# Performance work log

Hardware: AMD Instinct MI355X
Metric: run time of the kernel (lower is better)

The kernel has to match this reference:

```python
import jax, jax.numpy as jnp
import numpy as np
import math

H = 16
D_MODEL = 1024
LEN_Q = 2048
LEN_K = 2048
D_K = 64
D_V = 64
B = 4
NEG = -1000000000.0


def setup_inputs() -> dict:
    key = jax.random.key(0)
    ks = jax.random.split(key, 9)
    Q = jax.random.normal(ks[0], (B, LEN_Q, D_MODEL), dtype=jnp.float32)
    K = jax.random.normal(ks[1], (B, LEN_K, D_MODEL), dtype=jnp.float32)
    V = jax.random.normal(ks[2], (B, LEN_K, D_MODEL), dtype=jnp.float32)
    mask = jax.random.randint(ks[3], (B, LEN_K), 0, 2, dtype=jnp.int32)
    s = 1.0 / math.sqrt(D_MODEL)
    Wq = jax.random.normal(ks[4], (H * D_K, D_MODEL), dtype=jnp.float32) * s
    bq = jnp.zeros((H * D_K,), dtype=jnp.float32)
    Wk = jax.random.normal(ks[5], (H * D_K, D_MODEL), dtype=jnp.float32) * s
    Wv = jax.random.normal(ks[6], (H * D_V, D_MODEL), dtype=jnp.float32) * s
    bv = jnp.zeros((H * D_V,), dtype=jnp.float32)
    return {"Q": Q, "K": K, "V": V, "mask": mask,
            "Wq": Wq, "bq": bq, "Wk": Wk, "Wv": Wv, "bv": bv}


def reference(Q, K, V, mask, Wq, bq, Wk, Wv, bv):
    scale = math.sqrt(float(D_K))
    # projections (W_Q, W_V have bias; W_K does not)
    q = (jnp.einsum('bsd,od->bso', Q, Wq) + bq).reshape(B, LEN_Q, H, D_K)
    k = jnp.einsum('bsd,od->bso', K, Wk).reshape(B, LEN_K, H, D_K)
    v = (jnp.einsum('bsd,od->bso', V, Wv) + bv).reshape(B, LEN_K, H, D_V)
    # scores [B, H, len_q, len_k]
    A = jnp.einsum('bqhd,bkhd->bhqk', q, k) / scale
    m = (mask != 0)[:, None, None, :]  # [B,1,1,len_k]
    A = jnp.where(m, A, A + 0.0)
    A = jnp.where(m, A, NEG)
    alpha = jax.nn.softmax(A, axis=-1)
    out = jnp.einsum('bhqk,bkhd->bqhd', alpha, v)  # [B, len_q, H, d_v]
    return out.reshape(B, LEN_Q, H * D_V)
```

## Files before the change

### kernel.cpp

```cpp
#include <hip/hip_runtime.h>
#include <stdint.h>
#include <math.h>

#define NH 16
#define DM 1024
#define SEQ 2048
#define DH 64
#define NB 4
#define NEG2 (-1.4426950408889634e9f)
#define SCL2 (0.18033688011112042f)

typedef __attribute__((ext_vector_type(8))) short bf16x8;
typedef __attribute__((ext_vector_type(4))) short bf16x4;
typedef __attribute__((ext_vector_type(4))) float f32x4;
typedef unsigned short u16;
typedef uint32_t u32;

__device__ __forceinline__ u16 f2bf(float f) {
    union { float f; u32 i; } c; c.f = f;
    u32 r = c.i + 0x7fffu + ((c.i >> 16) & 1u);
    return (u16)(r >> 16);
}
__device__ __forceinline__ u32 packbf(float lo, float hi) {
    union { float f; u32 i; } a, b; a.f = lo; b.f = hi;
    return ((a.i + 0x8000u) >> 16) | ((b.i + 0x8000u) & 0xFFFF0000u);
}

__device__ __forceinline__ float fexp2(float x) {
#if __has_builtin(__builtin_amdgcn_exp2f)
    return __builtin_amdgcn_exp2f(x);
#else
    return exp2f(x);
#endif
}

__device__ __forceinline__ f32x4 pv_mfma(bf16x4 a, bf16x4 b, f32x4 c) {
#if __has_builtin(__builtin_amdgcn_mfma_f32_16x16x16bf16_1k)
    return __builtin_amdgcn_mfma_f32_16x16x16bf16_1k(a, b, c, 0, 0, 0);
#else
    f32x4 d;
    asm volatile("s_nop 1\n\t"
                 "v_mfma_f32_16x16x16_bf16 %0, %1, %2, %3\n\t"
                 "s_nop 7\n\t"
                 "s_nop 7"
                 : "=v"(d) : "v"(a), "v"(b), "v"(c));
    return d;
#endif
}

__global__ __launch_bounds__(256) void cvt_kernel(const float* __restrict__ src,
                                                  u16* __restrict__ dst, int n4) {
    int i = blockIdx.x * 256 + threadIdx.x;
    if (i >= n4) return;
    float4 v = ((const float4*)src)[i];
    ushort4 o = { f2bf(v.x), f2bf(v.y), f2bf(v.z), f2bf(v.w) };
    ((ushort4*)dst)[i] = o;
}

__global__ __launch_bounds__(256) void prep_kernel(
    const float* __restrict__ Wq, const float* __restrict__ Wk,
    const float* __restrict__ Wv, const int* __restrict__ mask,
    u16* __restrict__ wqb, u16* __restrict__ wkb, u16* __restrict__ wvb,
    float* __restrict__ mf) {
    const int bid = blockIdx.x;
    if (bid < 3072) {
        const float* src = (bid < 1024) ? Wq : (bid < 2048) ? Wk : Wv;
        u16* dst = (bid < 1024) ? wqb : (bid < 2048) ? wkb : wvb;
        int i = (bid & 1023) * 256 + threadIdx.x;
        float4 v = ((const float4*)src)[i];
        ushort4 o = { f2bf(v.x), f2bf(v.y), f2bf(v.z), f2bf(v.w) };
        ((ushort4*)dst)[i] = o;
    } else {
        int i = (bid - 3072) * 256 + threadIdx.x;
        mf[i] = mask[i] ? 0.0f : NEG2;
    }
}

__global__ __launch_bounds__(256, 3) void proj_kernel(
    const u16* __restrict__ X, const u16* __restrict__ W,
    const float* __restrict__ bias, u16* __restrict__ out, int vt)
{
    __shared__ __align__(16) u16 sbuf[2][8192];
    const int tid  = threadIdx.x;
    const int lane = tid & 63;
    const int wave = tid >> 6;
    const int row  = lane & 15;
    const int quad = lane >> 4;
    const int n0 = blockIdx.x * 128;
    const int m0 = blockIdx.y * 128;
    const int wm = (wave & 1) * 64;
    const int wn = (wave >> 1) * 64;

    const int srow = tid >> 2;
    const int sk8  = (tid & 3) * 8;
    const u16* xg = X + (size_t)(m0 + srow) * DM + sk8;
    const u16* wg = W + (size_t)(n0 + srow) * DM + sk8;
    const int ldsA = tid * 8;
    const int ldsB = 4096 + tid * 8;

    {
        uint4 a0 = *(const uint4*)(xg);
        uint4 a1 = *(const uint4*)(xg + (size_t)64 * DM);
        uint4 b0 = *(const uint4*)(wg);
        uint4 b1 = *(const uint4*)(wg + (size_t)64 * DM);
        *(uint4*)(&sbuf[0][ldsA])        = a0;
        *(uint4*)(&sbuf[0][ldsA + 2048]) = a1;
        *(uint4*)(&sbuf[0][ldsB])        = b0;
        *(uint4*)(&sbuf[0][ldsB + 2048]) = b1;
    }

    f32x4 acc[4][4] = {};
    for (int ki = 0; ki < 32; ++ki) {
        __syncthreads();
        const int ktn = (ki == 31) ? 0 : (ki + 1) * 32;
        uint4 a0 = *(const uint4*)(xg + ktn);
        uint4 a1 = *(const uint4*)(xg + (size_t)64 * DM + ktn);
        uint4 b0 = *(const uint4*)(wg + ktn);
        uint4 b1 = *(const uint4*)(wg + (size_t)64 * DM + ktn);

        const u16* Ab = sbuf[ki & 1];
        const u16* Bb = Ab + 4096;
        bf16x8 af[4], bf[4];
#pragma unroll
        for (int i = 0; i < 4; i++)
            af[i] = *(const bf16x8*)(Ab + (wm + i * 16 + row) * 32 + quad * 8);
#pragma unroll
        for (int j = 0; j < 4; j++)
            bf[j] = *(const bf16x8*)(Bb + (wn + j * 16 + row) * 32 + quad * 8);
#pragma unroll
        for (int i = 0; i < 4; i++)
#pragma unroll
            for (int j = 0; j < 4; j++)
                acc[i][j] = __builtin_amdgcn_mfma_f32_16x16x32_bf16(af[i], bf[j], acc[i][j], 0, 0, 0);

        u16* nb = sbuf[(ki + 1) & 1];
        *(uint4*)(nb + ldsA)        = a0;
        *(uint4*)(nb + ldsA + 2048) = a1;
        *(uint4*)(nb + ldsB)        = b0;
        *(uint4*)(nb + ldsB + 2048) = b1;
    }

    const int bidx = m0 >> 11;
#pragma unroll
    for (int j = 0; j < 4; j++) {
        const int n = n0 + wn + j * 16 + row;
        const int h = n >> 6;
        const int c = n & (DH - 1);
        const float bv = bias ? bias[n] : 0.0f;
#pragma unroll
        for (int i = 0; i < 4; i++) {
            const int mbase = m0 + wm + i * 16 + quad * 4;
            const int s = mbase & (SEQ - 1);
            if (vt) {
                ushort4 o = { f2bf(acc[i][j][0] + bv), f2bf(acc[i][j][1] + bv),
                              f2bf(acc[i][j][2] + bv), f2bf(acc[i][j][3] + bv) };
                size_t idx = (((size_t)(bidx * NH + h) * 32 + (s >> 6)) * DH + c) * 64 + (s & 63);
                *(ushort4*)(out + idx) = o;
            } else {
#pragma unroll
                for (int r = 0; r < 4; r++)
                    out[(size_t)((bidx * NH + h) * SEQ + s + r) * DH + c] = f2bf(acc[i][j][r] + bv);
            }
        }
    }
}

__global__ __launch_bounds__(256, 3) void attn_kernel(
    const u16* __restrict__ qws, const u16* __restrict__ kws,
    const u16* __restrict__ vws, const float* __restrict__ maskf,
    float* __restrict__ out)
{
    __shared__ __align__(16) u16 kbuf[2][64 * 72];
    __shared__ __align__(16) u16 vbuf[2][64 * 72];
    const int tid  = threadIdx.x;
    const int lane = tid & 63;
    const int wave = tid >> 6;
    const int row  = lane & 15;
    const int quad = lane >> 4;
    const int bid = blockIdx.x;
    const int qb = bid & 15;
    const int h  = (bid >> 4) & (NH - 1);
    const int b  = bid >> 8;
    const int q0 = qb * 128 + wave * 32;

    const u16* qbase = qws + (size_t)(b * NH + h) * SEQ * DH;
    const u16* kbase = kws + (size_t)(b * NH + h) * SEQ * DH;
    const u16* vtb   = vws + (size_t)(b * NH + h) * 32 * (DH * 64);
    const float* mrow = maskf + b * SEQ;

    const int srow = tid >> 3;
    const int scol = (tid & 7) * 8;
    const u16* kgp = kbase + (size_t)srow * DH + scol;
    const int ldso = srow * 72 + scol;
    const int vldso = ldso;

    bf16x8 qf[2][2];
#pragma unroll
    for (int gi = 0; gi < 2; gi++) {
        qf[gi][0] = *(const bf16x8*)(qbase + (size_t)(q0 + gi * 16 + row) * DH + quad * 8);
        qf[gi][1] = *(const bf16x8*)(qbase + (size_t)(q0 + gi * 16 + row) * DH + 32 + quad * 8);
    }

    f32x4 O[2][4] = {};
    float lrun[2] = {0.0f, 0.0f};

    {
        uint4 k0 = *(const uint4*)(kgp);
        uint4 k1 = *(const uint4*)(kgp + (size_t)32 * DH);
        uint4 v0 = *(const uint4*)(vtb + tid * 8);
        uint4 v1 = *(const uint4*)(vtb + (tid + 256) * 8);
        *(uint4*)(&kbuf[0][ldso])            = k0;
        *(uint4*)(&kbuf[0][32 * 72 + ldso])  = k1;
        *(uint4*)(&vbuf[0][vldso])           = v0;
        *(uint4*)(&vbuf[0][32 * 72 + vldso]) = v1;
    }

    for (int it = 0; it < 32; ++it) {
        const int kt = it * 64;
        __syncthreads();
        float4 mk[4];
#pragma unroll
        for (int g = 0; g < 4; g++)
            mk[g] = *(const float4*)(mrow + kt + g * 16 + quad * 4);
        const int itn = (it == 31) ? 0 : it + 1;
        uint4 kr0 = *(const uint4*)(kgp + (size_t)itn * 64 * DH);
        uint4 kr1 = *(const uint4*)(kgp + (size_t)(itn * 64 + 32) * DH);
        uint4 vr0 = *(const uint4*)(vtb + (size_t)itn * 4096 + tid * 8);
        uint4 vr1 = *(const uint4*)(vtb + (size_t)itn * 4096 + (tid + 256) * 8);

        const u16* kb = kbuf[it & 1];
        f32x4 st[2][4] = {};
#pragma unroll
        for (int g = 0; g < 4; g++) {
#pragma unroll
            for (int ks = 0; ks < 2; ks++) {
                bf16x8 kf = *(const bf16x8*)(kb + (g * 16 + row) * 72 + ks * 32 + quad * 8);
                st[0][g] = __builtin_amdgcn_mfma_f32_16x16x32_bf16(kf, qf[0][ks], st[0][g], 0, 0, 0);
                st[1][g] = __builtin_amdgcn_mfma_f32_16x16x32_bf16(kf, qf[1][ks], st[1][g], 0, 0, 0);
            }
        }

        union { u32 u[2]; bf16x4 v; } pw[2][4];
#pragma unroll
        for (int gi = 0; gi < 2; gi++) {
            float lsum = 0.0f;
#pragma unroll
            for (int g = 0; g < 4; g++) {
                float p0 = fexp2(fmaf(st[gi][g][0], SCL2, mk[g].x));
                float p1 = fexp2(fmaf(st[gi][g][1], SCL2, mk[g].y));
                float p2 = fexp2(fmaf(st[gi][g][2], SCL2, mk[g].z));
                float p3 = fexp2(fmaf(st[gi][g][3], SCL2, mk[g].w));
                lsum += (p0 + p1) + (p2 + p3);
                pw[gi][g].u[0] = packbf(p0, p1);
                pw[gi][g].u[1] = packbf(p2, p3);
            }
            lsum += __shfl_xor(lsum, 16, 64);
            lsum += __shfl_xor(lsum, 32, 64);
            lrun[gi] += lsum;
        }

        const u16* vb = vbuf[it & 1];
#pragma unroll
        for (int dg = 0; dg < 4; dg++) {
#pragma unroll
            for (int g = 0; g < 4; g++) {
                bf16x4 vfrag = *(const bf16x4*)(vb + (dg * 16 + row) * 72 + g * 16 + quad * 4);
                O[0][dg] = pv_mfma(vfrag, pw[0][g].v, O[0][dg]);
                O[1][dg] = pv_mfma(vfrag, pw[1][g].v, O[1][dg]);
            }
        }

        u16* nkb = kbuf[(it + 1) & 1];
        u16* nvb = vbuf[(it + 1) & 1];
        *(uint4*)(nkb + ldso)             = kr0;
        *(uint4*)(nkb + 32 * 72 + ldso)   = kr1;
        *(uint4*)(nvb + vldso)            = vr0;
        *(uint4*)(nvb + 32 * 72 + vldso)  = vr1;
    }

#pragma unroll
    for (int gi = 0; gi < 2; gi++) {
        const float rl = 1.0f / lrun[gi];
        const int q = q0 + gi * 16 + row;
#pragma unroll
        for (int dg = 0; dg < 4; dg++) {
            float4 o4 = { O[gi][dg][0] * rl, O[gi][dg][1] * rl,
                          O[gi][dg][2] * rl, O[gi][dg][3] * rl };
            *(float4*)(out + (size_t)(b * SEQ + q) * (NH * DH) + h * DH + dg * 16 + quad * 4) = o4;
        }
    }
}

extern "C" void kernel_launch(void* const* d_in, const int* in_sizes, int n_in,
                              void* d_out, int out_size, void* d_ws, size_t ws_size,
                              hipStream_t stream) {
    const float* Q    = (const float*)d_in[0];
    const float* K    = (const float*)d_in[1];
    const float* V    = (const float*)d_in[2];
    const int*   mask = (const int*)d_in[3];
    const float* Wq   = (const float*)d_in[4];
    const float* bq   = (const float*)d_in[5];
    const float* Wk   = (const float*)d_in[6];
    const float* Wv   = (const float*)d_in[7];
    const float* bv   = (const float*)d_in[8];
    float* out = (float*)d_out;

    const size_t XN = (size_t)NB * SEQ * DM;
    const size_t WN = (size_t)DM * DM;
    u16* ws = (u16*)d_ws;
    u16* xbuf = ws;
    u16* wqb  = ws + XN;
    u16* wkb  = wqb + WN;
    u16* wvb  = wkb + WN;
    u16* qws  = wvb + WN;
    u16* kws  = qws + XN;
    u16* vws  = kws + XN;
    float* maskf = (float*)(vws + XN);

    dim3 blk(256);
    const int gX = (int)(XN / 4 / 256);
    prep_kernel<<<3072 + 32, blk, 0, stream>>>(Wq, Wk, Wv, mask, wqb, wkb, wvb, maskf);

    dim3 pgrid(DM / 128, NB * SEQ / 128);
    cvt_kernel<<<gX, blk, 0, stream>>>(Q, xbuf, (int)(XN / 4));
    proj_kernel<<<pgrid, blk, 0, stream>>>(xbuf, wqb, bq, qws, 0);
    cvt_kernel<<<gX, blk, 0, stream>>>(K, xbuf, (int)(XN / 4));
    proj_kernel<<<pgrid, blk, 0, stream>>>(xbuf, wkb, nullptr, kws, 0);
    cvt_kernel<<<gX, blk, 0, stream>>>(V, xbuf, (int)(XN / 4));
    proj_kernel<<<pgrid, blk, 0, stream>>>(xbuf, wvb, bv, vws, 1);

    attn_kernel<<<dim3(NB * NH * (SEQ / 128)), blk, 0, stream>>>(qws, kws, vws, maskf, out);
}
```

Measured before the change: 360.0 us.

## Fuse fp32-to-bf16 conversion into a single batched QKV projection launch

```diff
diff --git a/kernel.cpp b/kernel.cpp
--- a/kernel.cpp
+++ b/kernel.cpp
@@ -20,6 +20,9 @@
     union { float f; u32 i; } c; c.f = f;
     u32 r = c.i + 0x7fffu + ((c.i >> 16) & 1u);
     return (u16)(r >> 16);
+}
+__device__ __forceinline__ u32 pk2(float lo, float hi) {
+    return (u32)f2bf(lo) | ((u32)f2bf(hi) << 16);
 }
 __device__ __forceinline__ u32 packbf(float lo, float hi) {
     union { float f; u32 i; } a, b; a.f = lo; b.f = hi;
@@ -46,15 +49,6 @@
                  : "=v"(d) : "v"(a), "v"(b), "v"(c));
     return d;
 #endif
-}
-
-__global__ __launch_bounds__(256) void cvt_kernel(const float* __restrict__ src,
-                                                  u16* __restrict__ dst, int n4) {
-    int i = blockIdx.x * 256 + threadIdx.x;
-    if (i >= n4) return;
-    float4 v = ((const float4*)src)[i];
-    ushort4 o = { f2bf(v.x), f2bf(v.y), f2bf(v.z), f2bf(v.w) };
-    ((ushort4*)dst)[i] = o;
 }
 
 __global__ __launch_bounds__(256) void prep_kernel(
@@ -77,34 +71,53 @@
 }
 
 __global__ __launch_bounds__(256, 3) void proj_kernel(
-    const u16* __restrict__ X, const u16* __restrict__ W,
-    const float* __restrict__ bias, u16* __restrict__ out, int vt)
+    const float* __restrict__ Qx, const float* __restrict__ Kx,
+    const float* __restrict__ Vx,
+    const u16* __restrict__ wqb, const u16* __restrict__ wkb,
+    const u16* __restrict__ wvb,
+    const float* __restrict__ bq, const float* __restrict__ bv,
+    u16* __restrict__ qo, u16* __restrict__ ko, u16* __restrict__ vo)
 {
     __shared__ __align__(16) u16 sbuf[2][8192];
+    const int which = blockIdx.y >> 6;
+    const float* X  = (which == 0) ? Qx : (which == 1) ? Kx : Vx;
+    const u16*   W  = (which == 0) ? wqb : (which == 1) ? wkb : wvb;
+    const float* bias = (which == 0) ? bq : (which == 2) ? bv : nullptr;
+    u16* out = (which == 0) ? qo : (which == 1) ? ko : vo;
+    const int vt = (which == 2);
+
     const int tid  = threadIdx.x;
     const int lane = tid & 63;
     const int wave = tid >> 6;
     const int row  = lane & 15;
     const int quad = lane >> 4;
     const int n0 = blockIdx.x * 128;
-    const int m0 = blockIdx.y * 128;
+    const int m0 = (blockIdx.y & 63) * 128;
     const int wm = (wave & 1) * 64;
     const int wn = (wave >> 1) * 64;
 
     const int srow = tid >> 2;
-    const int sk8  = (tid & 3) * 8;
-    const u16* xg = X + (size_t)(m0 + srow) * DM + sk8;
-    const u16* wg = W + (size_t)(n0 + srow) * DM + sk8;
-    const int ldsA = tid * 8;
-    const int ldsB = 4096 + tid * 8;
+    const int sch  = tid & 3;
+    const float* xg = X + (size_t)(m0 + srow) * DM + sch * 8;
+    const u16*   wg = W + (size_t)(n0 + srow) * DM + sch * 8;
+    const int swz   = (sch ^ ((srow >> 1) & 3)) * 8;
+    const int ldsA  = srow * 32 + swz;
+    const int ldsB  = 4096 + ldsA;
+    const int rsw   = (quad ^ ((row >> 1) & 3)) * 8;
 
     {
-        uint4 a0 = *(const uint4*)(xg);
-        uint4 a1 = *(const uint4*)(xg + (size_t)64 * DM);
+        float4 a00 = *(const float4*)(xg);
+        float4 a01 = *(const float4*)(xg + 4);
+        float4 a10 = *(const float4*)(xg + (size_t)64 * DM);
+        float4 a11 = *(const float4*)(xg + (size_t)64 * DM + 4);
         uint4 b0 = *(const uint4*)(wg);
         uint4 b1 = *(const uint4*)(wg + (size_t)64 * DM);
-        *(uint4*)(&sbuf[0][ldsA])        = a0;
-        *(uint4*)(&sbuf[0][ldsA + 2048]) = a1;
+        uint4 ac0 = { pk2(a00.x, a00.y), pk2(a00.z, a00.w),
+                      pk2(a01.x, a01.y), pk2(a01.z, a01.w) };
+        uint4 ac1 = { pk2(a10.x, a10.y), pk2(a10.z, a10.w),
+                      pk2(a11.x, a11.y), pk2(a11.z, a11.w) };
+        *(uint4*)(&sbuf[0][ldsA])        = ac0;
+        *(uint4*)(&sbuf[0][ldsA + 2048]) = ac1;
         *(uint4*)(&sbuf[0][ldsB])        = b0;
         *(uint4*)(&sbuf[0][ldsB + 2048]) = b1;
     }
@@ -113,29 +126,35 @@
     for (int ki = 0; ki < 32; ++ki) {
         __syncthreads();
         const int ktn = (ki == 31) ? 0 : (ki + 1) * 32;
-        uint4 a0 = *(const uint4*)(xg + ktn);
-        uint4 a1 = *(const uint4*)(xg + (size_t)64 * DM + ktn);
+        float4 a00 = *(const float4*)(xg + ktn);
+        float4 a01 = *(const float4*)(xg + ktn + 4);
+        float4 a10 = *(const float4*)(xg + (size_t)64 * DM + ktn);
+        float4 a11 = *(const float4*)(xg + (size_t)64 * DM + ktn + 4);
         uint4 b0 = *(const uint4*)(wg + ktn);
         uint4 b1 = *(const uint4*)(wg + (size_t)64 * DM + ktn);
 
         const u16* Ab = sbuf[ki & 1];
         const u16* Bb = Ab + 4096;
-        bf16x8 af[4], bf[4];
+        bf16x8 af[4], bfr[4];
 #pragma unroll
         for (int i = 0; i < 4; i++)
-            af[i] = *(const bf16x8*)(Ab + (wm + i * 16 + row) * 32 + quad * 8);
+            af[i] = *(const bf16x8*)(Ab + (wm + i * 16 + row) * 32 + rsw);
 #pragma unroll
         for (int j = 0; j < 4; j++)
-            bf[j] = *(const bf16x8*)(Bb + (wn + j * 16 + row) * 32 + quad * 8);
+            bfr[j] = *(const bf16x8*)(Bb + (wn + j * 16 + row) * 32 + rsw);
 #pragma unroll
         for (int i = 0; i < 4; i++)
 #pragma unroll
             for (int j = 0; j < 4; j++)
-                acc[i][j] = __builtin_amdgcn_mfma_f32_16x16x32_bf16(af[i], bf[j], acc[i][j], 0, 0, 0);
+                acc[i][j] = __builtin_amdgcn_mfma_f32_16x16x32_bf16(af[i], bfr[j], acc[i][j], 0, 0, 0);
 
         u16* nb = sbuf[(ki + 1) & 1];
-        *(uint4*)(nb + ldsA)        = a0;
-        *(uint4*)(nb + ldsA + 2048) = a1;
+        uint4 ac0 = { pk2(a00.x, a00.y), pk2(a00.z, a00.w),
+                      pk2(a01.x, a01.y), pk2(a01.z, a01.w) };
+        uint4 ac1 = { pk2(a10.x, a10.y), pk2(a10.z, a10.w),
+                      pk2(a11.x, a11.y), pk2(a11.z, a11.w) };
+        *(uint4*)(nb + ldsA)        = ac0;
+        *(uint4*)(nb + ldsA + 2048) = ac1;
         *(uint4*)(nb + ldsB)        = b0;
         *(uint4*)(nb + ldsB + 2048) = b1;
     }
@@ -146,20 +165,20 @@
         const int n = n0 + wn + j * 16 + row;
         const int h = n >> 6;
         const int c = n & (DH - 1);
-        const float bv = bias ? bias[n] : 0.0f;
+        const float bvv = bias ? bias[n] : 0.0f;
 #pragma unroll
         for (int i = 0; i < 4; i++) {
             const int mbase = m0 + wm + i * 16 + quad * 4;
             const int s = mbase & (SEQ - 1);
             if (vt) {
-                ushort4 o = { f2bf(acc[i][j][0] + bv), f2bf(acc[i][j][1] + bv),
-                              f2bf(acc[i][j][2] + bv), f2bf(acc[i][j][3] + bv) };
+                ushort4 o = { f2bf(acc[i][j][0] + bvv), f2bf(acc[i][j][1] + bvv),
+                              f2bf(acc[i][j][2] + bvv), f2bf(acc[i][j][3] + bvv) };
                 size_t idx = (((size_t)(bidx * NH + h) * 32 + (s >> 6)) * DH + c) * 64 + (s & 63);
                 *(ushort4*)(out + idx) = o;
             } else {
 #pragma unroll
                 for (int r = 0; r < 4; r++)
-                    out[(size_t)((bidx * NH + h) * SEQ + s + r) * DH + c] = f2bf(acc[i][j][r] + bv);
+                    out[(size_t)((bidx * NH + h) * SEQ + s + r) * DH + c] = f2bf(acc[i][j][r] + bvv);
             }
         }
     }
@@ -177,7 +196,8 @@
     const int wave = tid >> 6;
     const int row  = lane & 15;
     const int quad = lane >> 4;
-    const int bid = blockIdx.x;
+    const int bid0 = blockIdx.x;
+    const int bid  = ((bid0 & 7) << 7) | (bid0 >> 3);
     const int qb = bid & 15;
     const int h  = (bid >> 4) & (NH - 1);
     const int b  = bid >> 8;
@@ -308,8 +328,7 @@
     const size_t XN = (size_t)NB * SEQ * DM;
     const size_t WN = (size_t)DM * DM;
     u16* ws = (u16*)d_ws;
-    u16* xbuf = ws;
-    u16* wqb  = ws + XN;
+    u16* wqb  = ws;
     u16* wkb  = wqb + WN;
     u16* wvb  = wkb + WN;
     u16* qws  = wvb + WN;
@@ -318,16 +337,10 @@
     float* maskf = (float*)(vws + XN);
 
     dim3 blk(256);
-    const int gX = (int)(XN / 4 / 256);
     prep_kernel<<<3072 + 32, blk, 0, stream>>>(Wq, Wk, Wv, mask, wqb, wkb, wvb, maskf);
 
-    dim3 pgrid(DM / 128, NB * SEQ / 128);
-    cvt_kernel<<<gX, blk, 0, stream>>>(Q, xbuf, (int)(XN / 4));
-    proj_kernel<<<pgrid, blk, 0, stream>>>(xbuf, wqb, bq, qws, 0);
-    cvt_kernel<<<gX, blk, 0, stream>>>(K, xbuf, (int)(XN / 4));
-    proj_kernel<<<pgrid, blk, 0, stream>>>(xbuf, wkb, nullptr, kws, 0);
-    cvt_kernel<<<gX, blk, 0, stream>>>(V, xbuf, (int)(XN / 4));
-    proj_kernel<<<pgrid, blk, 0, stream>>>(xbuf, wvb, bv, vws, 1);
+    proj_kernel<<<dim3(DM / 128, 192), blk, 0, stream>>>(
+        Q, K, V, wqb, wkb, wvb, bq, bv, qws, kws, vws);
 
     attn_kernel<<<dim3(NB * NH * (SEQ / 128)), blk, 0, stream>>>(qws, kws, vws, maskf, out);
 }
```

New measurement: 374.6 us. 1.04x slower.

## Use direct global-to-LDS loads with swizzle and XCD-aware tile mapping in projection GEMM

Applied to the files above, without the earlier changes.

```diff
diff --git a/kernel.cpp b/kernel.cpp
--- a/kernel.cpp
+++ b/kernel.cpp
@@ -45,6 +45,16 @@
                  "s_nop 7"
                  : "=v"(d) : "v"(a), "v"(b), "v"(c));
     return d;
+#endif
+}
+
+__device__ __forceinline__ void gl_lds16(const u16* g, u16* l) {
+#if __has_builtin(__builtin_amdgcn_global_load_lds)
+    __builtin_amdgcn_global_load_lds(
+        (const __attribute__((address_space(1))) void*)g,
+        (__attribute__((address_space(3))) void*)l, 16, 0, 0);
+#else
+    *(uint4*)(l + (threadIdx.x & 63) * 8) = *(const uint4*)(g);
 #endif
 }
 
@@ -76,69 +86,67 @@
     }
 }
 
-__global__ __launch_bounds__(256, 3) void proj_kernel(
+__global__ __launch_bounds__(256, 4) void proj_kernel(
     const u16* __restrict__ X, const u16* __restrict__ W,
     const float* __restrict__ bias, u16* __restrict__ out, int vt)
 {
     __shared__ __align__(16) u16 sbuf[2][8192];
+    const int p   = blockIdx.y * 8 + blockIdx.x;
+    const int xcd = p & 7;
+    const int i8  = p >> 3;
+    const int ly  = xcd * 8 + (i8 >> 3);
+    const int lx  = i8 & 7;
+
     const int tid  = threadIdx.x;
     const int lane = tid & 63;
     const int wave = tid >> 6;
     const int row  = lane & 15;
     const int quad = lane >> 4;
-    const int n0 = blockIdx.x * 128;
-    const int m0 = blockIdx.y * 128;
+    const int n0 = lx * 128;
+    const int m0 = ly * 128;
     const int wm = (wave & 1) * 64;
     const int wn = (wave >> 1) * 64;
 
-    const int srow = tid >> 2;
-    const int sk8  = (tid & 3) * 8;
-    const u16* xg = X + (size_t)(m0 + srow) * DM + sk8;
-    const u16* wg = W + (size_t)(n0 + srow) * DM + sk8;
-    const int ldsA = tid * 8;
-    const int ldsB = 4096 + tid * 8;
-
-    {
-        uint4 a0 = *(const uint4*)(xg);
-        uint4 a1 = *(const uint4*)(xg + (size_t)64 * DM);
-        uint4 b0 = *(const uint4*)(wg);
-        uint4 b1 = *(const uint4*)(wg + (size_t)64 * DM);
-        *(uint4*)(&sbuf[0][ldsA])        = a0;
-        *(uint4*)(&sbuf[0][ldsA + 2048]) = a1;
-        *(uint4*)(&sbuf[0][ldsB])        = b0;
-        *(uint4*)(&sbuf[0][ldsB + 2048]) = b1;
-    }
+    const int r0 = wave * 16 + (lane >> 2);
+    const int c0 = (lane & 3) ^ ((r0 >> 1) & 3);
+    const u16* xg0 = X + (size_t)(m0 + r0) * DM + c0 * 8;
+    const u16* xg1 = xg0 + (size_t)64 * DM;
+    const u16* wg0 = W + (size_t)(n0 + r0) * DM + c0 * 8;
+    const u16* wg1 = wg0 + (size_t)64 * DM;
+    const int la0 = wave * 512;
+
+    const int rsw = (quad ^ ((row >> 1) & 3)) * 8;
+
+#define STAGE(bsel, kt) do {                         \
+        u16* ab = &sbuf[bsel][la0];                  \
+        gl_lds16(xg0 + (kt), ab);                    \
+        gl_lds16(xg1 + (kt), ab + 2048);             \
+        gl_lds16(wg0 + (kt), ab + 4096);             \
+        gl_lds16(wg1 + (kt), ab + 6144);             \
+    } while (0)
 
     f32x4 acc[4][4] = {};
+    STAGE(0, 0);
     for (int ki = 0; ki < 32; ++ki) {
         __syncthreads();
-        const int ktn = (ki == 31) ? 0 : (ki + 1) * 32;
-        uint4 a0 = *(const uint4*)(xg + ktn);
-        uint4 a1 = *(const uint4*)(xg + (size_t)64 * DM + ktn);
-        uint4 b0 = *(const uint4*)(wg + ktn);
-        uint4 b1 = *(const uint4*)(wg + (size_t)64 * DM + ktn);
+        if (ki < 31) STAGE((ki + 1) & 1, (ki + 1) * 32);
 
         const u16* Ab = sbuf[ki & 1];
         const u16* Bb = Ab + 4096;
-        bf16x8 af[4], bf[4];
+        bf16x8 af[4], bfr[4];
 #pragma unroll
         for (int i = 0; i < 4; i++)
-            af[i] = *(const bf16x8*)(Ab + (wm + i * 16 + row) * 32 + quad * 8);
+            af[i] = *(const bf16x8*)(Ab + (wm + i * 16 + row) * 32 + rsw);
 #pragma unroll
         for (int j = 0; j < 4; j++)
-            bf[j] = *(const bf16x8*)(Bb + (wn + j * 16 + row) * 32 + quad * 8);
+            bfr[j] = *(const bf16x8*)(Bb + (wn + j * 16 + row) * 32 + rsw);
 #pragma unroll
         for (int i = 0; i < 4; i++)
 #pragma unroll
             for (int j = 0; j < 4; j++)
-                acc[i][j] = __builtin_amdgcn_mfma_f32_16x16x32_bf16(af[i], bf[j], acc[i][j], 0, 0, 0);
-
-        u16* nb = sbuf[(ki + 1) & 1];
-        *(uint4*)(nb + ldsA)        = a0;
-        *(uint4*)(nb + ldsA + 2048) = a1;
-        *(uint4*)(nb + ldsB)        = b0;
-        *(uint4*)(nb + ldsB + 2048) = b1;
-    }
+                acc[i][j] = __builtin_amdgcn_mfma_f32_16x16x32_bf16(af[i], bfr[j], acc[i][j], 0, 0, 0);
+    }
+#undef STAGE
 
     const int bidx = m0 >> 11;
 #pragma unroll
@@ -146,20 +154,20 @@
         const int n = n0 + wn + j * 16 + row;
         const int h = n >> 6;
         const int c = n & (DH - 1);
-        const float bv = bias ? bias[n] : 0.0f;
+        const float bvv = bias ? bias[n] : 0.0f;
 #pragma unroll
         for (int i = 0; i < 4; i++) {
             const int mbase = m0 + wm + i * 16 + quad * 4;
             const int s = mbase & (SEQ - 1);
             if (vt) {
-                ushort4 o = { f2bf(acc[i][j][0] + bv), f2bf(acc[i][j][1] + bv),
-                              f2bf(acc[i][j][2] + bv), f2bf(acc[i][j][3] + bv) };
+                ushort4 o = { f2bf(acc[i][j][0] + bvv), f2bf(acc[i][j][1] + bvv),
+                              f2bf(acc[i][j][2] + bvv), f2bf(acc[i][j][3] + bvv) };
                 size_t idx = (((size_t)(bidx * NH + h) * 32 + (s >> 6)) * DH + c) * 64 + (s & 63);
                 *(ushort4*)(out + idx) = o;
             } else {
 #pragma unroll
                 for (int r = 0; r < 4; r++)
-                    out[(size_t)((bidx * NH + h) * SEQ + s + r) * DH + c] = f2bf(acc[i][j][r] + bv);
+                    out[(size_t)((bidx * NH + h) * SEQ + s + r) * DH + c] = f2bf(acc[i][j][r] + bvv);
             }
         }
     }
@@ -319,15 +327,16 @@
 
     dim3 blk(256);
     const int gX = (int)(XN / 4 / 256);
+    dim3 pgrid(DM / 128, NB * SEQ / 128);
+
     prep_kernel<<<3072 + 32, blk, 0, stream>>>(Wq, Wk, Wv, mask, wqb, wkb, wvb, maskf);
 
-    dim3 pgrid(DM / 128, NB * SEQ / 128);
-    cvt_kernel<<<gX, blk, 0, stream>>>(Q, xbuf, (int)(XN / 4));
-    proj_kernel<<<pgrid, blk, 0, stream>>>(xbuf, wqb, bq, qws, 0);
     cvt_kernel<<<gX, blk, 0, stream>>>(K, xbuf, (int)(XN / 4));
     proj_kernel<<<pgrid, blk, 0, stream>>>(xbuf, wkb, nullptr, kws, 0);
     cvt_kernel<<<gX, blk, 0, stream>>>(V, xbuf, (int)(XN / 4));
     proj_kernel<<<pgrid, blk, 0, stream>>>(xbuf, wvb, bv, vws, 1);
+    cvt_kernel<<<gX, blk, 0, stream>>>(Q, xbuf, (int)(XN / 4));
+    proj_kernel<<<pgrid, blk, 0, stream>>>(xbuf, wqb, bq, qws, 0);
 
     attn_kernel<<<dim3(NB * NH * (SEQ / 128)), blk, 0, stream>>>(qws, kws, vws, maskf, out);
 }
```

After: 339.6 us. -5.6%, faster.
